# Kernel optimization log

Measured on AMD Instinct MI355X. Metric: run time of the kernel, lower is better.

The kernel has to match this reference:

```python
import jax, jax.numpy as jnp
import numpy as np

B = 1024      # total windows (batch*windows_per_image)
W = 7         # window_size
T = W * W     # tokens per window = 49
C = 256       # scaled_emb_dim = emb_dim * 2**level
H = 8         # heads
D = C // H    # head_dim = 32
NUM_POS = 2 * W - 1


def _relative_pos():
    coords = np.arange(W)
    coords = np.stack(np.meshgrid(coords, coords, indexing='ij')).reshape(2, -1)
    rp = coords[:, :, None] - coords[:, None, :] + (W - 1)
    return jnp.asarray(rp, dtype=jnp.int32)  # (2, T, T)


def setup_inputs() -> dict:
    key = jax.random.key(0)
    ks = jax.random.split(key, 12)
    s = 0.02
    return {
        'x': jax.random.normal(ks[0], (B, T, C), dtype=jnp.float32),
        'relative_pos': _relative_pos(),
        'bias_table': jax.random.truncated_normal(ks[1], -2.0, 2.0, (H, NUM_POS, NUM_POS), dtype=jnp.float32) * s,
        'wq': jax.random.normal(ks[2], (C, H, D), dtype=jnp.float32) / np.sqrt(C),
        'bq': jnp.zeros((H, D), dtype=jnp.float32),
        'wk': jax.random.normal(ks[3], (C, H, D), dtype=jnp.float32) / np.sqrt(C),
        'bk': jnp.zeros((H, D), dtype=jnp.float32),
        'wv': jax.random.normal(ks[4], (C, H, D), dtype=jnp.float32) / np.sqrt(C),
        'bv': jnp.zeros((H, D), dtype=jnp.float32),
        'wo': jax.random.normal(ks[5], (H, D, C), dtype=jnp.float32) / np.sqrt(C),
        'bo': jnp.zeros((C,), dtype=jnp.float32),
        'dw': jax.random.normal(ks[6], (C, C), dtype=jnp.float32) / np.sqrt(C),
        'db': jnp.zeros((C,), dtype=jnp.float32),
    }


def reference(x, relative_pos, bias_table, wq, bq, wk, bk, wv, bv, wo, bo, dw, db):
    # QKV projections (flax DenseGeneral with bias)
    q = jnp.einsum('btc,chd->bthd', x, wq) + bq  # (B,T,H,D)
    k = jnp.einsum('btc,chd->bthd', x, wk) + bk
    v = jnp.einsum('btc,chd->bthd', x, wv) + bv

    # gathered relative position bias: (H, T, T)
    bias = bias_table[:, relative_pos[0], relative_pos[1]]

    # attention logits with query scaling (flax dot_product_attention)
    q = q / jnp.sqrt(jnp.asarray(D, dtype=q.dtype))
    logits = jnp.einsum('bqhd,bkhd->bhqk', q, k) + bias[None]
    attn = jax.nn.softmax(logits, axis=-1)

    out = jnp.einsum('bhqk,bkhd->bqhd', attn, v)
    y = jnp.einsum('bqhd,hdc->bqc', out, wo) + bo  # attention out projection
    y = jnp.einsum('btc,cf->btf', y, dw) + db      # trailing Dense(scaled_emb_dim)
    return y
```

## Files before the change

### kernel.cpp

```cpp
#include <hip/hip_runtime.h>
#include <stdint.h>

#define T 49
#define CCH 256

typedef __bf16 bf16x8 __attribute__((ext_vector_type(8)));
typedef float f32x4 __attribute__((ext_vector_type(4)));

static __device__ __forceinline__ unsigned short f2bf(float f){
  __bf16 h = (__bf16)f;
  return __builtin_bit_cast(unsigned short, h);
}
static __device__ __forceinline__ float bf2f(unsigned short h){
  return __builtin_bit_cast(float, ((uint32_t)h) << 16);
}
static __device__ __forceinline__ uint32_t pk2(float a, float b){
  return (uint32_t)f2bf(a) | ((uint32_t)f2bf(b) << 16);
}
static __device__ __forceinline__ f32x4 mfma16(bf16x8 a, bf16x8 b, f32x4 c){
  return __builtin_amdgcn_mfma_f32_16x16x32_bf16(a, b, c, 0, 0, 0);
}
#define SWZ(row) ((((row) & 7) << 4))

static __device__ __forceinline__ bf16x8 build_frag(uint32_t lo_w0, uint32_t lo_w1,
                                                    uint32_t hi_w0, uint32_t hi_w1,
                                                    int srcA, int srcB, bool use_hi){
  uint32_t a0 = (uint32_t)__shfl((int)lo_w0, srcA, 64);
  uint32_t c0 = (uint32_t)__shfl((int)hi_w0, srcA, 64);
  uint32_t a1 = (uint32_t)__shfl((int)lo_w1, srcA, 64);
  uint32_t c1 = (uint32_t)__shfl((int)hi_w1, srcA, 64);
  uint32_t a2 = (uint32_t)__shfl((int)lo_w0, srcB, 64);
  uint32_t c2 = (uint32_t)__shfl((int)hi_w0, srcB, 64);
  uint32_t a3 = (uint32_t)__shfl((int)lo_w1, srcB, 64);
  uint32_t c3 = (uint32_t)__shfl((int)hi_w1, srcB, 64);
  uint4 u = use_hi ? make_uint4(c0, c1, c2, c3) : make_uint4(a0, a1, a2, a3);
  return __builtin_bit_cast(bf16x8, u);
}


__global__ void prep_wqkvT(const float* __restrict__ wq, const float* __restrict__ wk,
                           const float* __restrict__ wv, unsigned short* __restrict__ out){
  int bk = blockIdx.x;
  int p = bk >> 8, kk = bk & 255;
  int n = threadIdx.x;
  const float* w = (p == 0) ? wq : (p == 1 ? wk : wv);
  float scl = (p == 0) ? 0.17677669529663687f : 1.0f;
  out[(size_t)(p * 256 + n) * 256 + kk] = f2bf(w[kk * 256 + n] * scl);
}

__global__ void prep_wodT(const float* __restrict__ wo, const float* __restrict__ dw,
                          unsigned short* __restrict__ out){
  int hd = blockIdx.x;
  int c = threadIdx.x;
  float s = 0.f;
  for (int cp = 0; cp < 256; ++cp) s = fmaf(wo[hd * 256 + cp], dw[cp * 256 + c], s);
  out[(size_t)c * 256 + hd] = f2bf(s);
}

__global__ void prep_misc(const int* __restrict__ rp, const float* __restrict__ btab,
                          const float* __restrict__ bq, const float* __restrict__ bk,
                          const float* __restrict__ bv, const float* __restrict__ bo,
                          const float* __restrict__ dwm, const float* __restrict__ db,
                          unsigned short* __restrict__ biasP, float* __restrict__ bqkv,
                          float* __restrict__ bod){
  int t = threadIdx.x;
  if (blockIdx.x == 0){
    for (int idx = t; idx < 768; idx += 256){
      int p = idx >> 8, n = idx & 255;
      float v = (p == 0) ? bq[n] * 0.17677669529663687f : (p == 1 ? bk[n] : bv[n]);
      bqkv[idx] = v;
    }
    float s = db[t];
    for (int cp = 0; cp < 256; ++cp) s = fmaf(bo[cp], dwm[cp * 256 + t], s);
    bod[t] = s;
  } else {
    int h = blockIdx.x - 1;
    for (int idx = t; idx < 4096; idx += 256){
      int r  = idx & 3;
      int lo = (idx >> 2) & 15;
      int g  = (idx >> 6) & 3;
      int nt = (idx >> 8) & 3;
      int jt = idx >> 10;
      int j = 16 * jt + 4 * g + r;
      int i = 16 * nt + lo;
      float v;
      if (j >= T) v = -1e30f;
      else if (i >= T) v = 0.f;
      else {
        int r0 = rp[i * 49 + j];
        int r1 = rp[2401 + i * 49 + j];
        v = btab[h * 169 + r0 * 13 + r1];
      }
      biasP[h * 4096 + idx] = f2bf(v);
    }
  }
}

__launch_bounds__(512, 4)
__global__ void wmsa_main(const float* __restrict__ x,
                          const unsigned short* __restrict__ wqkvT,
                          const unsigned short* __restrict__ wodT,
                          const unsigned short* __restrict__ biasP,
                          const float* __restrict__ bqkv,
                          const float* __restrict__ bod,
                          float* __restrict__ y){
  __shared__ unsigned short xs[64 * 256];
  __shared__ unsigned short vts[8 * 32 * 64];

  const int b    = blockIdx.x;
  const int tid  = threadIdx.x;
  const int h    = tid >> 6;
  const int lane = tid & 63;
  const int g    = lane >> 4;
  const int lo   = lane & 15;
  char* xs_c  = (char*)xs;
  char* vts_c = (char*)vts;

  const float* xbp = x + (size_t)b * T * CCH;
  {
    float4 vv[8];
    #pragma unroll
    for (int k2 = 0; k2 < 8; ++k2){
      int idx = tid + k2 * 512;
      int row = idx >> 6, c4 = idx & 63;
      vv[k2] = make_float4(0.f, 0.f, 0.f, 0.f);
      if (row < T) vv[k2] = reinterpret_cast<const float4*>(xbp)[row * 64 + c4];
    }
    #pragma unroll
    for (int k2 = 0; k2 < 8; ++k2){
      int idx = tid + k2 * 512;
      int row = idx >> 6, c4 = idx & 63;
      *reinterpret_cast<uint2*>(xs_c + row * 512 + ((c4 * 8) ^ SWZ(row)))
          = make_uint2(pk2(vv[k2].x, vv[k2].y), pk2(vv[k2].z, vv[k2].w));
    }
  }
  __syncthreads();

  const int  swz  = (lo & 7) << 4;
  const int  lo3  = lo & 3;
  const int  gq   = g >> 1;
  const int  gh   = (g & 1) * 8;
  const int  srcA = lo + 16 * ((2 * g) & 3);
  const int  srcB = lo + 16 * ((2 * g + 1) & 3);
  const bool ghi  = (g >= 2);

  const char* xb0 = xs_c + lo * 512 + ((16 * g) ^ swz);
  const char* xb1 = xs_c + lo * 512 + ((64 + 16 * g) ^ swz);
  const char* vr = vts_c + h * 4096 + lo * 128 + ((g ^ lo3) * 16);

  bf16x8 fk[4], fq[4];

  {
    const char* wv0 = (const char*)wqkvT + (size_t)(512 + h * 32 + lo) * 512 + 16 * g;
    const char* wv1 = wv0 + 16 * 512;
    f32x4 acc[4][2];
    #pragma unroll
    for (int mt = 0; mt < 4; ++mt)
      #pragma unroll
      for (int nt = 0; nt < 2; ++nt) acc[mt][nt] = f32x4{0,0,0,0};

    #pragma unroll 1
    for (int kb = 0; kb < 2; ++kb){
      const char* p0 = xb0 + kb * 256;
      const char* p1 = xb1 + kb * 256;
      const char* w0 = wv0 + kb * 256;
      const char* w1 = wv1 + kb * 256;
      bf16x8 wf[2][4];
      #pragma unroll
      for (int q = 0; q < 4; ++q){
        wf[0][q] = *reinterpret_cast<const bf16x8*>(w0 + q * 64);
        wf[1][q] = *reinterpret_cast<const bf16x8*>(w1 + q * 64);
      }
      #pragma unroll
      for (int q = 0; q < 4; ++q){
        bf16x8 ax[4];
        #pragma unroll
        for (int mt = 0; mt < 4; ++mt)
          ax[mt] = *reinterpret_cast<const bf16x8*>(((q & 1) ? p1 : p0) + mt * 8192 + (q >> 1) * 128);
        #pragma unroll
        for (int nt = 0; nt < 2; ++nt)
          #pragma unroll
          for (int mt = 0; mt < 4; ++mt) acc[mt][nt] = mfma16(ax[mt], wf[nt][q], acc[mt][nt]);
      }
    }
    char* vw = vts_c + h * 4096 + lo * 128 + gh;
    #pragma unroll
    for (int nt = 0; nt < 2; ++nt){
      const float bvs = bqkv[512 + h * 32 + 16 * nt + lo];
      #pragma unroll
      for (int mt = 0; mt < 4; ++mt){
        f32x4 t = acc[mt][nt];
        *reinterpret_cast<uint2*>(vw + nt * 2048 + (((2 * mt + gq) ^ lo3) * 16))
            = make_uint2(pk2(t[0] + bvs, t[1] + bvs), pk2(t[2] + bvs, t[3] + bvs));
      }
    }
  }

  {
    const char* wk0 = (const char*)wqkvT + (size_t)(256 + h * 32 + lo) * 512 + 16 * g;
    const char* wk1 = wk0 + 16 * 512;
    f32x4 acc[2][4];
    #pragma unroll
    for (int mt = 0; mt < 2; ++mt)
      #pragma unroll
      for (int nt = 0; nt < 4; ++nt) acc[mt][nt] = f32x4{0,0,0,0};

    #pragma unroll 1
    for (int kb = 0; kb < 2; ++kb){
      const char* p0 = xb0 + kb * 256;
      const char* p1 = xb1 + kb * 256;
      const char* w0 = wk0 + kb * 256;
      const char* w1 = wk1 + kb * 256;
      bf16x8 wf[2][4];
      #pragma unroll
      for (int q = 0; q < 4; ++q){
        wf[0][q] = *reinterpret_cast<const bf16x8*>(w0 + q * 64);
        wf[1][q] = *reinterpret_cast<const bf16x8*>(w1 + q * 64);
      }
      #pragma unroll
      for (int q = 0; q < 4; ++q){
        bf16x8 bx[4];
        #pragma unroll
        for (int nt = 0; nt < 4; ++nt)
          bx[nt] = *reinterpret_cast<const bf16x8*>(((q & 1) ? p1 : p0) + nt * 8192 + (q >> 1) * 128);
        #pragma unroll
        for (int mt = 0; mt < 2; ++mt)
          #pragma unroll
          for (int nt = 0; nt < 4; ++nt) acc[mt][nt] = mfma16(wf[mt][q], bx[nt], acc[mt][nt]);
      }
    }
    uint32_t pkk[2][4][2];
    #pragma unroll
    for (int mt = 0; mt < 2; ++mt){
      const float4 b4 = *reinterpret_cast<const float4*>(bqkv + 256 + h * 32 + 16 * mt + 4 * g);
      #pragma unroll
      for (int nt = 0; nt < 4; ++nt){
        f32x4 t = acc[mt][nt];
        t[0] += b4.x; t[1] += b4.y; t[2] += b4.z; t[3] += b4.w;
        pkk[mt][nt][0] = pk2(t[0], t[1]); pkk[mt][nt][1] = pk2(t[2], t[3]);
      }
    }
    #pragma unroll
    for (int nt = 0; nt < 4; ++nt)
      fk[nt] = build_frag(pkk[0][nt][0], pkk[0][nt][1], pkk[1][nt][0], pkk[1][nt][1], srcA, srcB, ghi);
  }

  {
    const char* wq0 = (const char*)wqkvT + (size_t)(h * 32 + lo) * 512 + 16 * g;
    const char* wq1 = wq0 + 16 * 512;
    f32x4 acc[2][4];
    #pragma unroll
    for (int mt = 0; mt < 2; ++mt)
      #pragma unroll
      for (int nt = 0; nt < 4; ++nt) acc[mt][nt] = f32x4{0,0,0,0};

    #pragma unroll 1
    for (int kb = 0; kb < 2; ++kb){
      const char* p0 = xb0 + kb * 256;
      const char* p1 = xb1 + kb * 256;
      const char* w0 = wq0 + kb * 256;
      const char* w1 = wq1 + kb * 256;
      bf16x8 wf[2][4];
      #pragma unroll
      for (int q = 0; q < 4; ++q){
        wf[0][q] = *reinterpret_cast<const bf16x8*>(w0 + q * 64);
        wf[1][q] = *reinterpret_cast<const bf16x8*>(w1 + q * 64);
      }
      #pragma unroll
      for (int q = 0; q < 4; ++q){
        bf16x8 bx[4];
        #pragma unroll
        for (int nt = 0; nt < 4; ++nt)
          bx[nt] = *reinterpret_cast<const bf16x8*>(((q & 1) ? p1 : p0) + nt * 8192 + (q >> 1) * 128);
        #pragma unroll
        for (int mt = 0; mt < 2; ++mt)
          #pragma unroll
          for (int nt = 0; nt < 4; ++nt) acc[mt][nt] = mfma16(wf[mt][q], bx[nt], acc[mt][nt]);
      }
    }
    uint32_t pq[2][4][2];
    #pragma unroll
    for (int mt = 0; mt < 2; ++mt){
      const float4 b4 = *reinterpret_cast<const float4*>(bqkv + h * 32 + 16 * mt + 4 * g);
      #pragma unroll
      for (int nt = 0; nt < 4; ++nt){
        f32x4 t = acc[mt][nt];
        t[0] += b4.x; t[1] += b4.y; t[2] += b4.z; t[3] += b4.w;
        pq[mt][nt][0] = pk2(t[0], t[1]); pq[mt][nt][1] = pk2(t[2], t[3]);
      }
    }
    #pragma unroll
    for (int nt = 0; nt < 4; ++nt)
      fq[nt] = build_frag(pq[0][nt][0], pq[0][nt][1], pq[1][nt][0], pq[1][nt][1], srcA, srcB, ghi);
  }
  __syncthreads();

  bf16x8 av[2][2];
  #pragma unroll
  for (int dt = 0; dt < 2; ++dt)
    #pragma unroll
    for (int ktj = 0; ktj < 2; ++ktj)
      av[dt][ktj] = *reinterpret_cast<const bf16x8*>(vr + dt * 2048 + ktj * 64);

  const char* bbase0 = (const char*)biasP + h * 8192 + (g * 16 + lo) * 8;
  const char* bbase1 = bbase0 + 4096;
  const int oslot0 = ((h * 4 + gq) ^ (lo & 7)) * 16;
  const int oslot1 = ((h * 4 + 2 + gq) ^ (lo & 7)) * 16;
  char* ow = xs_c + lo * 512 + gh;

  #pragma unroll 1
  for (int nt = 0; nt < 4; ++nt){
    const char* bn0 = bbase0 + nt * 512;
    const char* bn1 = bbase1 + nt * 512;
    uint2 bb[4];
    bb[0] = *reinterpret_cast<const uint2*>(bn0);
    bb[1] = *reinterpret_cast<const uint2*>(bn0 + 2048);
    bb[2] = *reinterpret_cast<const uint2*>(bn1);
    bb[3] = *reinterpret_cast<const uint2*>(bn1 + 2048);
    f32x4 lacc[4];
    #pragma unroll
    for (int jt = 0; jt < 4; ++jt){
      lacc[jt] = mfma16(fk[jt], fq[nt], f32x4{0,0,0,0});
      lacc[jt][0] += bf2f((unsigned short)(bb[jt].x & 0xffff));
      lacc[jt][1] += bf2f((unsigned short)(bb[jt].x >> 16));
      lacc[jt][2] += bf2f((unsigned short)(bb[jt].y & 0xffff));
      lacc[jt][3] += bf2f((unsigned short)(bb[jt].y >> 16));
    }
    float m01a = fmaxf(fmaxf(lacc[0][0], lacc[0][1]), fmaxf(lacc[0][2], lacc[0][3]));
    float m01b = fmaxf(fmaxf(lacc[1][0], lacc[1][1]), fmaxf(lacc[1][2], lacc[1][3]));
    float m23a = fmaxf(fmaxf(lacc[2][0], lacc[2][1]), fmaxf(lacc[2][2], lacc[2][3]));
    float m23b = fmaxf(fmaxf(lacc[3][0], lacc[3][1]), fmaxf(lacc[3][2], lacc[3][3]));
    float m = fmaxf(fmaxf(m01a, m01b), fmaxf(m23a, m23b));
    m = fmaxf(m, __shfl_xor(m, 16, 64));
    m = fmaxf(m, __shfl_xor(m, 32, 64));
    float ssum = 0.f;
    uint32_t pw[4][2];
    #pragma unroll
    for (int jt = 0; jt < 4; ++jt){
      f32x4 t = lacc[jt];
      #pragma unroll
      for (int r = 0; r < 4; ++r){
        t[r] = exp2f((t[r] - m) * 1.4426950408889634f);
        ssum += t[r];
      }
      pw[jt][0] = pk2(t[0], t[1]);
      pw[jt][1] = pk2(t[2], t[3]);
    }
    ssum += __shfl_xor(ssum, 16, 64);
    ssum += __shfl_xor(ssum, 32, 64);
    const float r0 = 1.f / ssum;

    bf16x8 pf0 = build_frag(pw[0][0], pw[0][1], pw[1][0], pw[1][1], srcA, srcB, ghi);
    bf16x8 pf1 = build_frag(pw[2][0], pw[2][1], pw[3][0], pw[3][1], srcA, srcB, ghi);

    f32x4 o0 = mfma16(av[0][0], pf0, f32x4{0,0,0,0});
    o0 = mfma16(av[0][1], pf1, o0);
    f32x4 o1 = mfma16(av[1][0], pf0, f32x4{0,0,0,0});
    o1 = mfma16(av[1][1], pf1, o1);
    *reinterpret_cast<uint2*>(ow + nt * 8192 + oslot0)
        = make_uint2(pk2(o0[0] * r0, o0[1] * r0), pk2(o0[2] * r0, o0[3] * r0));
    *reinterpret_cast<uint2*>(ow + nt * 8192 + oslot1)
        = make_uint2(pk2(o1[0] * r0, o1[1] * r0), pk2(o1[2] * r0, o1[3] * r0));
  }
  __syncthreads();

  {
    const char* wo0 = (const char*)wodT + (size_t)(h * 32 + lo) * 512 + 16 * g;
    const char* wo1 = wo0 + 16 * 512;
    f32x4 facc[4][2];
    #pragma unroll
    for (int mt = 0; mt < 4; ++mt)
      #pragma unroll
      for (int nt = 0; nt < 2; ++nt) facc[mt][nt] = f32x4{0,0,0,0};

    #pragma unroll 1
    for (int kb = 0; kb < 2; ++kb){
      const char* p0 = xb0 + kb * 256;
      const char* p1 = xb1 + kb * 256;
      const char* w0 = wo0 + kb * 256;
      const char* w1 = wo1 + kb * 256;
      bf16x8 wf[2][4];
      #pragma unroll
      for (int q = 0; q < 4; ++q){
        wf[0][q] = *reinterpret_cast<const bf16x8*>(w0 + q * 64);
        wf[1][q] = *reinterpret_cast<const bf16x8*>(w1 + q * 64);
      }
      #pragma unroll
      for (int q = 0; q < 4; ++q){
        bf16x8 a[4];
        #pragma unroll
        for (int mt = 0; mt < 4; ++mt)
          a[mt] = *reinterpret_cast<const bf16x8*>(((q & 1) ? p1 : p0) + mt * 8192 + (q >> 1) * 128);
        #pragma unroll
        for (int nt = 0; nt < 2; ++nt)
          #pragma unroll
          for (int mt = 0; mt < 4; ++mt) facc[mt][nt] = mfma16(a[mt], wf[nt][q], facc[mt][nt]);
      }
    }
    #pragma unroll
    for (int nt = 0; nt < 2; ++nt){
      const int c = h * 32 + nt * 16 + lo;
      const float bd = bod[c];
      float* yb = y + (size_t)b * T * CCH + c;
      #pragma unroll
      for (int mt = 0; mt < 4; ++mt)
        #pragma unroll
        for (int r = 0; r < 4; ++r){
          int i = 16 * mt + 4 * g + r;
          if (i < T) yb[(size_t)i * CCH] = facc[mt][nt][r] + bd;
        }
    }
  }
}

extern "C" void kernel_launch(void* const* d_in, const int* in_sizes, int n_in,
                              void* d_out, int out_size, void* d_ws, size_t ws_size,
                              hipStream_t stream){
  const float* x    = (const float*)d_in[0];
  const int*   rp   = (const int*)d_in[1];
  const float* btab = (const float*)d_in[2];
  const float* wq   = (const float*)d_in[3];
  const float* bq   = (const float*)d_in[4];
  const float* wk   = (const float*)d_in[5];
  const float* bk   = (const float*)d_in[6];
  const float* wv   = (const float*)d_in[7];
  const float* bv   = (const float*)d_in[8];
  const float* wo   = (const float*)d_in[9];
  const float* bo   = (const float*)d_in[10];
  const float* dw   = (const float*)d_in[11];
  const float* db   = (const float*)d_in[12];
  float* y = (float*)d_out;

  char* ws = (char*)d_ws;
  unsigned short* wqkvT = (unsigned short*)(ws);
  unsigned short* wodT  = (unsigned short*)(ws + 393216);
  unsigned short* biasP = (unsigned short*)(ws + 524288);
  float* bqkv           = (float*)(ws + 589824);
  float* bod            = (float*)(ws + 592896);

  prep_wqkvT<<<768, 256, 0, stream>>>(wq, wk, wv, wqkvT);
  prep_wodT<<<256, 256, 0, stream>>>(wo, dw, wodT);
  prep_misc<<<9, 256, 0, stream>>>(rp, btab, bq, bk, bv, bo, dw, db, biasP, bqkv, bod);
  wmsa_main<<<1024, 512, 0, stream>>>(x, wqkvT, wodT, biasP, bqkv, bod, y);
}
```

Measured before the change: 136.2 us.

## Keep V in registers via shuffles, prefetch weights, store bias as fp32

The V projection result is no longer staged in shared memory. It is turned into MFMA fragments in registers with lane shuffles, which removes the vts buffer and its LDS traffic. K and output-projection weights are now prefetched into registers before the barriers, and the Q and V weight loads are software-pipelined one step ahead. The relative-position bias is stored as fp32 so the bf16 unpacking goes away, and the row max uses three-input max ops. In exchange, register pressure rises considerably under the 512-thread, 4-block launch bounds, which may cause spills.

Result: slower. 294.5 us (+116.2%).

```diff
diff --git a/kernel.cpp b/kernel.cpp
--- a/kernel.cpp
+++ b/kernel.cpp
@@ -11,14 +11,14 @@
   __bf16 h = (__bf16)f;
   return __builtin_bit_cast(unsigned short, h);
 }
-static __device__ __forceinline__ float bf2f(unsigned short h){
-  return __builtin_bit_cast(float, ((uint32_t)h) << 16);
-}
 static __device__ __forceinline__ uint32_t pk2(float a, float b){
   return (uint32_t)f2bf(a) | ((uint32_t)f2bf(b) << 16);
 }
 static __device__ __forceinline__ f32x4 mfma16(bf16x8 a, bf16x8 b, f32x4 c){
   return __builtin_amdgcn_mfma_f32_16x16x32_bf16(a, b, c, 0, 0, 0);
+}
+static __device__ __forceinline__ float max3f(float a, float b, float c){
+  return fmaxf(fmaxf(a, b), c);
 }
 #define SWZ(row) ((((row) & 7) << 4))
 
@@ -61,7 +61,7 @@
                           const float* __restrict__ bq, const float* __restrict__ bk,
                           const float* __restrict__ bv, const float* __restrict__ bo,
                           const float* __restrict__ dwm, const float* __restrict__ db,
-                          unsigned short* __restrict__ biasP, float* __restrict__ bqkv,
+                          float* __restrict__ biasF, float* __restrict__ bqkv,
                           float* __restrict__ bod){
   int t = threadIdx.x;
   if (blockIdx.x == 0){
@@ -91,7 +91,7 @@
         int r1 = rp[2401 + i * 49 + j];
         v = btab[h * 169 + r0 * 13 + r1];
       }
-      biasP[h * 4096 + idx] = f2bf(v);
+      biasF[h * 4096 + idx] = v;
     }
   }
 }
@@ -100,12 +100,11 @@
 __global__ void wmsa_main(const float* __restrict__ x,
                           const unsigned short* __restrict__ wqkvT,
                           const unsigned short* __restrict__ wodT,
-                          const unsigned short* __restrict__ biasP,
+                          const float* __restrict__ biasF,
                           const float* __restrict__ bqkv,
                           const float* __restrict__ bod,
                           float* __restrict__ y){
   __shared__ unsigned short xs[64 * 256];
-  __shared__ unsigned short vts[8 * 32 * 64];
 
   const int b    = blockIdx.x;
   const int tid  = threadIdx.x;
@@ -113,8 +112,26 @@
   const int lane = tid & 63;
   const int g    = lane >> 4;
   const int lo   = lane & 15;
-  char* xs_c  = (char*)xs;
-  char* vts_c = (char*)vts;
+  char* xs_c = (char*)xs;
+
+  const int  swz  = (lo & 7) << 4;
+  const int  gq   = g >> 1;
+  const int  gh   = (g & 1) * 8;
+  const int  srcA = lo + 16 * ((2 * g) & 3);
+  const int  srcB = lo + 16 * ((2 * g + 1) & 3);
+  const bool ghi  = (g >= 2);
+
+  const char* xb0 = xs_c + lo * 512 + ((16 * g) ^ swz);
+  const char* xb1 = xs_c + lo * 512 + ((64 + 16 * g) ^ swz);
+
+  const char* wk0 = (const char*)wqkvT + (size_t)(256 + h * 32 + lo) * 512 + 16 * g;
+  const char* wk1 = wk0 + 16 * 512;
+  const char* wq0 = (const char*)wqkvT + (size_t)(h * 32 + lo) * 512 + 16 * g;
+  const char* wq1 = wq0 + 16 * 512;
+  const char* wv0 = (const char*)wqkvT + (size_t)(512 + h * 32 + lo) * 512 + 16 * g;
+  const char* wv1 = wv0 + 16 * 512;
+  const char* wo0 = (const char*)wodT + (size_t)(h * 32 + lo) * 512 + 16 * g;
+  const char* wo1 = wo0 + 16 * 512;
 
   const float* xbp = x + (size_t)b * T * CCH;
   {
@@ -134,99 +151,40 @@
           = make_uint2(pk2(vv[k2].x, vv[k2].y), pk2(vv[k2].z, vv[k2].w));
     }
   }
+
+  bf16x8 kw0[8], kw1[8];
+  #pragma unroll
+  for (int kt = 0; kt < 8; ++kt){
+    kw0[kt] = *reinterpret_cast<const bf16x8*>(wk0 + kt * 64);
+    kw1[kt] = *reinterpret_cast<const bf16x8*>(wk1 + kt * 64);
+  }
   __syncthreads();
 
-  const int  swz  = (lo & 7) << 4;
-  const int  lo3  = lo & 3;
-  const int  gq   = g >> 1;
-  const int  gh   = (g & 1) * 8;
-  const int  srcA = lo + 16 * ((2 * g) & 3);
-  const int  srcB = lo + 16 * ((2 * g + 1) & 3);
-  const bool ghi  = (g >= 2);
-
-  const char* xb0 = xs_c + lo * 512 + ((16 * g) ^ swz);
-  const char* xb1 = xs_c + lo * 512 + ((64 + 16 * g) ^ swz);
-  const char* vr = vts_c + h * 4096 + lo * 128 + ((g ^ lo3) * 16);
-
-  bf16x8 fk[4], fq[4];
+  bf16x8 fk[4], fq[4], av[2][2];
 
   {
-    const char* wv0 = (const char*)wqkvT + (size_t)(512 + h * 32 + lo) * 512 + 16 * g;
-    const char* wv1 = wv0 + 16 * 512;
-    f32x4 acc[4][2];
-    #pragma unroll
-    for (int mt = 0; mt < 4; ++mt)
-      #pragma unroll
-      for (int nt = 0; nt < 2; ++nt) acc[mt][nt] = f32x4{0,0,0,0};
+    f32x4 acc[2][4];
+    #pragma unroll
+    for (int mt = 0; mt < 2; ++mt)
+      #pragma unroll
+      for (int nt = 0; nt < 4; ++nt) acc[mt][nt] = f32x4{0,0,0,0};
 
     #pragma unroll 1
     for (int kb = 0; kb < 2; ++kb){
-      const char* p0 = xb0 + kb * 256;
-      const char* p1 = xb1 + kb * 256;
-      const char* w0 = wv0 + kb * 256;
-      const char* w1 = wv1 + kb * 256;
-      bf16x8 wf[2][4];
       #pragma unroll
       for (int q = 0; q < 4; ++q){
-        wf[0][q] = *reinterpret_cast<const bf16x8*>(w0 + q * 64);
-        wf[1][q] = *reinterpret_cast<const bf16x8*>(w1 + q * 64);
-      }
-      #pragma unroll
-      for (int q = 0; q < 4; ++q){
-        bf16x8 ax[4];
-        #pragma unroll
-        for (int mt = 0; mt < 4; ++mt)
-          ax[mt] = *reinterpret_cast<const bf16x8*>(((q & 1) ? p1 : p0) + mt * 8192 + (q >> 1) * 128);
-        #pragma unroll
-        for (int nt = 0; nt < 2; ++nt)
-          #pragma unroll
-          for (int mt = 0; mt < 4; ++mt) acc[mt][nt] = mfma16(ax[mt], wf[nt][q], acc[mt][nt]);
-      }
-    }
-    char* vw = vts_c + h * 4096 + lo * 128 + gh;
-    #pragma unroll
-    for (int nt = 0; nt < 2; ++nt){
-      const float bvs = bqkv[512 + h * 32 + 16 * nt + lo];
-      #pragma unroll
-      for (int mt = 0; mt < 4; ++mt){
-        f32x4 t = acc[mt][nt];
-        *reinterpret_cast<uint2*>(vw + nt * 2048 + (((2 * mt + gq) ^ lo3) * 16))
-            = make_uint2(pk2(t[0] + bvs, t[1] + bvs), pk2(t[2] + bvs, t[3] + bvs));
-      }
-    }
-  }
-
-  {
-    const char* wk0 = (const char*)wqkvT + (size_t)(256 + h * 32 + lo) * 512 + 16 * g;
-    const char* wk1 = wk0 + 16 * 512;
-    f32x4 acc[2][4];
-    #pragma unroll
-    for (int mt = 0; mt < 2; ++mt)
-      #pragma unroll
-      for (int nt = 0; nt < 4; ++nt) acc[mt][nt] = f32x4{0,0,0,0};
-
-    #pragma unroll 1
-    for (int kb = 0; kb < 2; ++kb){
-      const char* p0 = xb0 + kb * 256;
-      const char* p1 = xb1 + kb * 256;
-      const char* w0 = wk0 + kb * 256;
-      const char* w1 = wk1 + kb * 256;
-      bf16x8 wf[2][4];
-      #pragma unroll
-      for (int q = 0; q < 4; ++q){
-        wf[0][q] = *reinterpret_cast<const bf16x8*>(w0 + q * 64);
-        wf[1][q] = *reinterpret_cast<const bf16x8*>(w1 + q * 64);
-      }
-      #pragma unroll
-      for (int q = 0; q < 4; ++q){
+        const int kt = kb * 4 + q;
+        const char* xb = (kt & 1) ? xb1 : xb0;
+        const int  im  = (kt >> 1) * 128;
         bf16x8 bx[4];
         #pragma unroll
         for (int nt = 0; nt < 4; ++nt)
-          bx[nt] = *reinterpret_cast<const bf16x8*>(((q & 1) ? p1 : p0) + nt * 8192 + (q >> 1) * 128);
+          bx[nt] = *reinterpret_cast<const bf16x8*>(xb + nt * 8192 + im);
         #pragma unroll
-        for (int mt = 0; mt < 2; ++mt)
-          #pragma unroll
-          for (int nt = 0; nt < 4; ++nt) acc[mt][nt] = mfma16(wf[mt][q], bx[nt], acc[mt][nt]);
+        for (int nt = 0; nt < 4; ++nt){
+          acc[0][nt] = mfma16(kw0[kt], bx[nt], acc[0][nt]);
+          acc[1][nt] = mfma16(kw1[kt], bx[nt], acc[1][nt]);
+        }
       }
     }
     uint32_t pkk[2][4][2];
@@ -246,37 +204,43 @@
   }
 
   {
-    const char* wq0 = (const char*)wqkvT + (size_t)(h * 32 + lo) * 512 + 16 * g;
-    const char* wq1 = wq0 + 16 * 512;
     f32x4 acc[2][4];
     #pragma unroll
     for (int mt = 0; mt < 2; ++mt)
       #pragma unroll
       for (int nt = 0; nt < 4; ++nt) acc[mt][nt] = f32x4{0,0,0,0};
 
+    bf16x8 wE0 = *reinterpret_cast<const bf16x8*>(wq0);
+    bf16x8 wE1 = *reinterpret_cast<const bf16x8*>(wq1);
+    bf16x8 wO0 = *reinterpret_cast<const bf16x8*>(wq0 + 64);
+    bf16x8 wO1 = *reinterpret_cast<const bf16x8*>(wq1 + 64);
+
     #pragma unroll 1
-    for (int kb = 0; kb < 2; ++kb){
-      const char* p0 = xb0 + kb * 256;
-      const char* p1 = xb1 + kb * 256;
-      const char* w0 = wq0 + kb * 256;
-      const char* w1 = wq1 + kb * 256;
-      bf16x8 wf[2][4];
-      #pragma unroll
-      for (int q = 0; q < 4; ++q){
-        wf[0][q] = *reinterpret_cast<const bf16x8*>(w0 + q * 64);
-        wf[1][q] = *reinterpret_cast<const bf16x8*>(w1 + q * 64);
-      }
-      #pragma unroll
-      for (int q = 0; q < 4; ++q){
-        bf16x8 bx[4];
-        #pragma unroll
-        for (int nt = 0; nt < 4; ++nt)
-          bx[nt] = *reinterpret_cast<const bf16x8*>(((q & 1) ? p1 : p0) + nt * 8192 + (q >> 1) * 128);
-        #pragma unroll
-        for (int mt = 0; mt < 2; ++mt)
-          #pragma unroll
-          for (int nt = 0; nt < 4; ++nt) acc[mt][nt] = mfma16(wf[mt][q], bx[nt], acc[mt][nt]);
-      }
+    for (int kp = 0; kp < 4; ++kp){
+      const int nb = (kp < 3) ? (kp * 128 + 128) : 0;
+      bf16x8 nE0 = *reinterpret_cast<const bf16x8*>(wq0 + nb);
+      bf16x8 nE1 = *reinterpret_cast<const bf16x8*>(wq1 + nb);
+      bf16x8 nO0 = *reinterpret_cast<const bf16x8*>(wq0 + nb + 64);
+      bf16x8 nO1 = *reinterpret_cast<const bf16x8*>(wq1 + nb + 64);
+      const int im = kp * 128;
+      bf16x8 bx[4];
+      #pragma unroll
+      for (int nt = 0; nt < 4; ++nt)
+        bx[nt] = *reinterpret_cast<const bf16x8*>(xb0 + nt * 8192 + im);
+      #pragma unroll
+      for (int nt = 0; nt < 4; ++nt){
+        acc[0][nt] = mfma16(wE0, bx[nt], acc[0][nt]);
+        acc[1][nt] = mfma16(wE1, bx[nt], acc[1][nt]);
+      }
+      #pragma unroll
+      for (int nt = 0; nt < 4; ++nt)
+        bx[nt] = *reinterpret_cast<const bf16x8*>(xb1 + nt * 8192 + im);
+      #pragma unroll
+      for (int nt = 0; nt < 4; ++nt){
+        acc[0][nt] = mfma16(wO0, bx[nt], acc[0][nt]);
+        acc[1][nt] = mfma16(wO1, bx[nt], acc[1][nt]);
+      }
+      wE0 = nE0; wE1 = nE1; wO0 = nO0; wO1 = nO1;
     }
     uint32_t pq[2][4][2];
     #pragma unroll
@@ -293,46 +257,97 @@
     for (int nt = 0; nt < 4; ++nt)
       fq[nt] = build_frag(pq[0][nt][0], pq[0][nt][1], pq[1][nt][0], pq[1][nt][1], srcA, srcB, ghi);
   }
+
+  {
+    f32x4 acc[4][2];
+    #pragma unroll
+    for (int mt = 0; mt < 4; ++mt)
+      #pragma unroll
+      for (int nt = 0; nt < 2; ++nt) acc[mt][nt] = f32x4{0,0,0,0};
+
+    bf16x8 wE0 = *reinterpret_cast<const bf16x8*>(wv0);
+    bf16x8 wE1 = *reinterpret_cast<const bf16x8*>(wv1);
+    bf16x8 wO0 = *reinterpret_cast<const bf16x8*>(wv0 + 64);
+    bf16x8 wO1 = *reinterpret_cast<const bf16x8*>(wv1 + 64);
+
+    #pragma unroll 1
+    for (int kp = 0; kp < 4; ++kp){
+      const int nb = (kp < 3) ? (kp * 128 + 128) : 0;
+      bf16x8 nE0 = *reinterpret_cast<const bf16x8*>(wv0 + nb);
+      bf16x8 nE1 = *reinterpret_cast<const bf16x8*>(wv1 + nb);
+      bf16x8 nO0 = *reinterpret_cast<const bf16x8*>(wv0 + nb + 64);
+      bf16x8 nO1 = *reinterpret_cast<const bf16x8*>(wv1 + nb + 64);
+      const int im = kp * 128;
+      bf16x8 ax[4];
+      #pragma unroll
+      for (int mt = 0; mt < 4; ++mt)
+        ax[mt] = *reinterpret_cast<const bf16x8*>(xb0 + mt * 8192 + im);
+      #pragma unroll
+      for (int mt = 0; mt < 4; ++mt){
+        acc[mt][0] = mfma16(ax[mt], wE0, acc[mt][0]);
+        acc[mt][1] = mfma16(ax[mt], wE1, acc[mt][1]);
+      }
+      #pragma unroll
+      for (int mt = 0; mt < 4; ++mt)
+        ax[mt] = *reinterpret_cast<const bf16x8*>(xb1 + mt * 8192 + im);
+      #pragma unroll
+      for (int mt = 0; mt < 4; ++mt){
+        acc[mt][0] = mfma16(ax[mt], wO0, acc[mt][0]);
+        acc[mt][1] = mfma16(ax[mt], wO1, acc[mt][1]);
+      }
+      wE0 = nE0; wE1 = nE1; wO0 = nO0; wO1 = nO1;
+    }
+    uint32_t pv[4][2][2];
+    #pragma unroll
+    for (int nt = 0; nt < 2; ++nt){
+      const float bvs = bqkv[512 + h * 32 + 16 * nt + lo];
+      #pragma unroll
+      for (int mt = 0; mt < 4; ++mt){
+        f32x4 t = acc[mt][nt];
+        t[0] += bvs; t[1] += bvs; t[2] += bvs; t[3] += bvs;
+        pv[mt][nt][0] = pk2(t[0], t[1]); pv[mt][nt][1] = pk2(t[2], t[3]);
+      }
+    }
+    #pragma unroll
+    for (int dt = 0; dt < 2; ++dt)
+      #pragma unroll
+      for (int ktj = 0; ktj < 2; ++ktj)
+        av[dt][ktj] = build_frag(pv[2 * ktj][dt][0], pv[2 * ktj][dt][1],
+                                 pv[2 * ktj + 1][dt][0], pv[2 * ktj + 1][dt][1],
+                                 srcA, srcB, ghi);
+  }
   __syncthreads();
 
-  bf16x8 av[2][2];
-  #pragma unroll
-  for (int dt = 0; dt < 2; ++dt)
-    #pragma unroll
-    for (int ktj = 0; ktj < 2; ++ktj)
-      av[dt][ktj] = *reinterpret_cast<const bf16x8*>(vr + dt * 2048 + ktj * 64);
-
-  const char* bbase0 = (const char*)biasP + h * 8192 + (g * 16 + lo) * 8;
-  const char* bbase1 = bbase0 + 4096;
+  const float* bfb = biasF + h * 4096 + (g * 16 + lo) * 4;
   const int oslot0 = ((h * 4 + gq) ^ (lo & 7)) * 16;
   const int oslot1 = ((h * 4 + 2 + gq) ^ (lo & 7)) * 16;
   char* ow = xs_c + lo * 512 + gh;
 
   #pragma unroll 1
   for (int nt = 0; nt < 4; ++nt){
-    const char* bn0 = bbase0 + nt * 512;
-    const char* bn1 = bbase1 + nt * 512;
-    uint2 bb[4];
-    bb[0] = *reinterpret_cast<const uint2*>(bn0);
-    bb[1] = *reinterpret_cast<const uint2*>(bn0 + 2048);
-    bb[2] = *reinterpret_cast<const uint2*>(bn1);
-    bb[3] = *reinterpret_cast<const uint2*>(bn1 + 2048);
+    const float* bf = bfb + nt * 256;
+    const float4 b0 = *reinterpret_cast<const float4*>(bf);
+    const float4 b1 = *reinterpret_cast<const float4*>(bf + 1024);
+    const float4 b2 = *reinterpret_cast<const float4*>(bf + 2048);
+    const float4 b3 = *reinterpret_cast<const float4*>(bf + 3072);
     f32x4 lacc[4];
     #pragma unroll
-    for (int jt = 0; jt < 4; ++jt){
+    for (int jt = 0; jt < 4; ++jt)
       lacc[jt] = mfma16(fk[jt], fq[nt], f32x4{0,0,0,0});
-      lacc[jt][0] += bf2f((unsigned short)(bb[jt].x & 0xffff));
-      lacc[jt][1] += bf2f((unsigned short)(bb[jt].x >> 16));
-      lacc[jt][2] += bf2f((unsigned short)(bb[jt].y & 0xffff));
-      lacc[jt][3] += bf2f((unsigned short)(bb[jt].y >> 16));
-    }
-    float m01a = fmaxf(fmaxf(lacc[0][0], lacc[0][1]), fmaxf(lacc[0][2], lacc[0][3]));
-    float m01b = fmaxf(fmaxf(lacc[1][0], lacc[1][1]), fmaxf(lacc[1][2], lacc[1][3]));
-    float m23a = fmaxf(fmaxf(lacc[2][0], lacc[2][1]), fmaxf(lacc[2][2], lacc[2][3]));
-    float m23b = fmaxf(fmaxf(lacc[3][0], lacc[3][1]), fmaxf(lacc[3][2], lacc[3][3]));
-    float m = fmaxf(fmaxf(m01a, m01b), fmaxf(m23a, m23b));
+    lacc[0][0] += b0.x; lacc[0][1] += b0.y; lacc[0][2] += b0.z; lacc[0][3] += b0.w;
+    lacc[1][0] += b1.x; lacc[1][1] += b1.y; lacc[1][2] += b1.z; lacc[1][3] += b1.w;
+    lacc[2][0] += b2.x; lacc[2][1] += b2.y; lacc[2][2] += b2.z; lacc[2][3] += b2.w;
+    lacc[3][0] += b3.x; lacc[3][1] += b3.y; lacc[3][2] += b3.z; lacc[3][3] += b3.w;
+
+    float t0 = max3f(lacc[0][0], lacc[0][1], lacc[0][2]);
+    float t1 = max3f(lacc[0][3], lacc[1][0], lacc[1][1]);
+    float t2 = max3f(lacc[1][2], lacc[1][3], lacc[2][0]);
+    float t3 = max3f(lacc[2][1], lacc[2][2], lacc[2][3]);
+    float t4 = max3f(lacc[3][0], lacc[3][1], lacc[3][2]);
+    float m  = fmaxf(max3f(t0, t1, t2), max3f(t3, t4, lacc[3][3]));
     m = fmaxf(m, __shfl_xor(m, 16, 64));
     m = fmaxf(m, __shfl_xor(m, 32, 64));
+
     float ssum = 0.f;
     uint32_t pw[4][2];
     #pragma unroll
@@ -362,11 +377,16 @@
     *reinterpret_cast<uint2*>(ow + nt * 8192 + oslot1)
         = make_uint2(pk2(o1[0] * r0, o1[1] * r0), pk2(o1[2] * r0, o1[3] * r0));
   }
+
+  bf16x8 fw0[8], fw1[8];
+  #pragma unroll
+  for (int kt = 0; kt < 8; ++kt){
+    fw0[kt] = *reinterpret_cast<const bf16x8*>(wo0 + kt * 64);
+    fw1[kt] = *reinterpret_cast<const bf16x8*>(wo1 + kt * 64);
+  }
   __syncthreads();
 
   {
-    const char* wo0 = (const char*)wodT + (size_t)(h * 32 + lo) * 512 + 16 * g;
-    const char* wo1 = wo0 + 16 * 512;
     f32x4 facc[4][2];
     #pragma unroll
     for (int mt = 0; mt < 4; ++mt)
@@ -375,26 +395,20 @@
 
     #pragma unroll 1
     for (int kb = 0; kb < 2; ++kb){
-      const char* p0 = xb0 + kb * 256;
-      const char* p1 = xb1 + kb * 256;
-      const char* w0 = wo0 + kb * 256;
-      const char* w1 = wo1 + kb * 256;
-      bf16x8 wf[2][4];
       #pragma unroll
       for (int q = 0; q < 4; ++q){
-        wf[0][q] = *reinterpret_cast<const bf16x8*>(w0 + q * 64);
-        wf[1][q] = *reinterpret_cast<const bf16x8*>(w1 + q * 64);
-      }
-      #pragma unroll
-      for (int q = 0; q < 4; ++q){
+        const int kt = kb * 4 + q;
+        const char* xb = (kt & 1) ? xb1 : xb0;
+        const int  im  = (kt >> 1) * 128;
         bf16x8 a[4];
         #pragma unroll
         for (int mt = 0; mt < 4; ++mt)
-          a[mt] = *reinterpret_cast<const bf16x8*>(((q & 1) ? p1 : p0) + mt * 8192 + (q >> 1) * 128);
+          a[mt] = *reinterpret_cast<const bf16x8*>(xb + mt * 8192 + im);
         #pragma unroll
-        for (int nt = 0; nt < 2; ++nt)
-          #pragma unroll
-          for (int mt = 0; mt < 4; ++mt) facc[mt][nt] = mfma16(a[mt], wf[nt][q], facc[mt][nt]);
+        for (int mt = 0; mt < 4; ++mt){
+          facc[mt][0] = mfma16(a[mt], fw0[kt], facc[mt][0]);
+          facc[mt][1] = mfma16(a[mt], fw1[kt], facc[mt][1]);
+        }
       }
     }
     #pragma unroll
@@ -434,12 +448,12 @@
   char* ws = (char*)d_ws;
   unsigned short* wqkvT = (unsigned short*)(ws);
   unsigned short* wodT  = (unsigned short*)(ws + 393216);
-  unsigned short* biasP = (unsigned short*)(ws + 524288);
-  float* bqkv           = (float*)(ws + 589824);
-  float* bod            = (float*)(ws + 592896);
+  float* biasF          = (float*)(ws + 524288);
+  float* bqkv           = (float*)(ws + 655360);
+  float* bod            = (float*)(ws + 658432);
 
   prep_wqkvT<<<768, 256, 0, stream>>>(wq, wk, wv, wqkvT);
   prep_wodT<<<256, 256, 0, stream>>>(wo, dw, wodT);
-  prep_misc<<<9, 256, 0, stream>>>(rp, btab, bq, bk, bv, bo, dw, db, biasP, bqkv, bod);
-  wmsa_main<<<1024, 512, 0, stream>>>(x, wqkvT, wodT, biasP, bqkv, bod, y);
-}
+  prep_misc<<<9, 256, 0, stream>>>(rp, btab, bq, bk, bv, bo, dw, db, biasF, bqkv, bod);
+  wmsa_main<<<1024, 512, 0, stream>>>(x, wqkvT, wodT, biasF, bqkv, bod, y);
+}
```
